# Performance work log

Hardware: AMD Instinct MI355X
Metric: run time of the kernel (lower is better)

The kernel has to match this reference:

```python
import jax, jax.numpy as jnp
import numpy as np

B, CDD, HIS, S, L, F, K = 32, 5, 100, 20, 3, 150, 18
NNEWS, RDIM = 10000, 256


def _maxpool3(x):
    # kernel [3,3,3], stride [3,3,3], no padding (torch MaxPool3d default)
    return jax.lax.reduce_window(x, -jnp.inf, jax.lax.max,
                                 (1, 1, 3, 3, 3), (1, 1, 3, 3, 3), 'VALID')


def setup_inputs() -> dict:
    key = jax.random.key(0)
    ks = jax.random.split(key, 10)
    return {
        'cdd_id': jax.random.randint(ks[0], (B, CDD), 0, NNEWS),
        'his_id': jax.random.randint(ks[1], (B, HIS), 0, NNEWS),
        'news_repr_table': jax.random.normal(ks[2], (NNEWS, RDIM), jnp.float32),
        'news_embedding_table': jax.random.normal(ks[3], (NNEWS, S * L * F), jnp.float32),
        'conv1_w': jax.random.normal(ks[4], (32, 3, 3, 3, 3), jnp.float32) * 0.1,
        'conv1_b': jax.random.normal(ks[5], (32,), jnp.float32) * 0.1,
        'conv2_w': jax.random.normal(ks[6], (16, 32, 3, 3, 3), jnp.float32) * 0.1,
        'conv2_b': jax.random.normal(ks[7], (16,), jnp.float32) * 0.1,
        'ltr_w': jax.random.normal(ks[8], (1, 128), jnp.float32) * 0.1,
        'ltr_b': jax.random.normal(ks[9], (1,), jnp.float32) * 0.1,
    }


def reference(cdd_id, his_id, news_repr_table, news_embedding_table,
              conv1_w, conv1_b, conv2_w, conv2_b, ltr_w, ltr_b):
    cdd_repr = news_repr_table[cdd_id]                    # [B,CDD,R]
    his_repr = news_repr_table[his_id]                    # [B,HIS,R]
    cdd_emb = news_embedding_table[cdd_id].reshape(B, CDD, S, L, F)
    his_emb = news_embedding_table[his_id]                # [B,HIS,S*L*F]

    # attention scores; original applies softmax then sorts the (detached)
    # weights -- softmax is monotone per row so argsort on logits is identical
    attn = jnp.einsum('bcr,bhr->bch', cdd_repr, his_repr)  # [B,CDD,HIS]
    topk_idx = jnp.argsort(-attn, axis=-1)[..., :K]        # [B,CDD,K]

    # direct gather (replaces the one_hot @ embedding matmul, same math)
    his_act = his_emb[jnp.arange(B)[:, None, None], topk_idx]  # [B,CDD,K,S*L*F]
    his_act = his_act.reshape(B, CDD, K, S, L, F)

    # fusion tensor at each dilation level
    cdd_t = cdd_emb.transpose(0, 1, 3, 2, 4)       # [B,CDD,L,S,F]
    his_t = his_act.transpose(0, 1, 2, 4, 3, 5)    # [B,CDD,K,L,S,F]
    fusion = jnp.einsum('bclsf,bckltf->bcklst', cdd_t, his_t) / np.sqrt(F).astype(np.float32)
    x = fusion.reshape(B * CDD, K, L, S, S).transpose(0, 2, 1, 3, 4)  # [B*CDD,L,K,S,S]

    dn = ('NCDHW', 'OIDHW', 'NCDHW')
    pad1 = [(1, 1)] * 3
    x = jax.lax.conv_general_dilated(x, conv1_w, (1, 1, 1), pad1, dimension_numbers=dn)
    x = jax.nn.relu(x + conv1_b[None, :, None, None, None])
    x = _maxpool3(x)                                # [B*CDD,32,6,6,6]
    x = jax.lax.conv_general_dilated(x, conv2_w, (1, 1, 1), pad1, dimension_numbers=dn)
    x = jax.nn.relu(x + conv2_b[None, :, None, None, None])
    x = _maxpool3(x)                                # [B*CDD,16,2,2,2]

    feat = x.reshape(B, CDD, -1)                    # [B,CDD,128]
    score = jnp.einsum('bcd,od->bco', feat, ltr_w)[..., 0] + ltr_b[0]  # [B,CDD]
    return jax.nn.log_softmax(score, axis=1)
```

## Files before the change

### kernel.cpp

```cpp
#include <hip/hip_runtime.h>
#include <hip/hip_bf16.h>
#include <math.h>

#define B_    32
#define CDD_  5
#define HIS_  100
#define S_    20
#define L_    3
#define F_    150
#define K_    18
#define RDIM_ 256
#define ROWE_ 9000
#define NBC_  160

__global__ __launch_bounds__(64) void attn_topk_kernel(
    const int* __restrict__ cdd_id, const int* __restrict__ his_id,
    const float* __restrict__ repr, int* __restrict__ gid,
    float* __restrict__ score) {
  int bc = blockIdx.x;
  int b  = bc / CDD_;
  int lane = threadIdx.x;
  __shared__ float cddv[RDIM_];
  int cid = cdd_id[bc];
  for (int i = lane; i < RDIM_; i += 64)
    cddv[i] = repr[(size_t)cid * RDIM_ + i];
  __syncthreads();

  float v0 = -INFINITY, v1 = -INFINITY;
  {
    const float* row = repr + (size_t)his_id[b * HIS_ + lane] * RDIM_;
    float acc = 0.f;
    for (int r = 0; r < RDIM_; r++) acc = fmaf(cddv[r], row[r], acc);
    v0 = acc;
  }
  if (lane + 64 < HIS_) {
    const float* row = repr + (size_t)his_id[b * HIS_ + lane + 64] * RDIM_;
    float acc = 0.f;
    for (int r = 0; r < RDIM_; r++) acc = fmaf(cddv[r], row[r], acc);
    v1 = acc;
  }

  for (int k = 0; k < K_; k++) {
    float bv; int bi;
    if (v1 > v0) { bv = v1; bi = lane + 64; } else { bv = v0; bi = lane; }
    #pragma unroll
    for (int off = 32; off >= 1; off >>= 1) {
      float ov = __shfl_xor(bv, off);
      int   oi = __shfl_xor(bi, off);
      if (ov > bv || (ov == bv && oi < bi)) { bv = ov; bi = oi; }
    }
    if (lane == 0) gid[bc * K_ + k] = his_id[b * HIS_ + bi];
    if (bi == lane)      v0 = -INFINITY;
    if (bi == lane + 64) v1 = -INFINITY;
  }
  if (lane == 0) score[bc] = 0.f;
}

__global__ __launch_bounds__(256) void fusion_kernel(
    const int* __restrict__ cdd_id, const int* __restrict__ gid,
    const float* __restrict__ emb, float* __restrict__ x1) {
  int bck = blockIdx.x;
  int bc = bck / K_, k = bck % K_;
  __shared__ float hs[ROWE_];
  const float* crow = emb + (size_t)cdd_id[bc] * ROWE_;
  const float4* h4 = (const float4*)(emb + (size_t)gid[bck] * ROWE_);
  float4* hs4 = (float4*)hs;
  for (int i = threadIdx.x; i < ROWE_ / 4; i += 256) hs4[i] = h4[i];
  __syncthreads();

  const float scale = 0.0816496580927726f;
  for (int tile = threadIdx.x; tile < 300; tile += 256) {
    int l = tile / 100; int rem = tile % 100;
    int s0 = (rem / 10) * 2, t0 = (rem % 10) * 2;
    const float* c0 = crow + s0 * 450 + l * 150;
    const float* c1 = c0 + 450;
    const float* h0 = hs + t0 * 450 + l * 150;
    const float* h1 = h0 + 450;
    float a00 = 0, a01 = 0, a10 = 0, a11 = 0;
    for (int f = 0; f < F_; f += 2) {
      float2 ca = *(const float2*)(c0 + f);
      float2 cb = *(const float2*)(c1 + f);
      float2 ha = *(const float2*)(h0 + f);
      float2 hb = *(const float2*)(h1 + f);
      a00 = fmaf(ca.x, ha.x, a00); a00 = fmaf(ca.y, ha.y, a00);
      a01 = fmaf(ca.x, hb.x, a01); a01 = fmaf(ca.y, hb.y, a01);
      a10 = fmaf(cb.x, ha.x, a10); a10 = fmaf(cb.y, ha.y, a10);
      a11 = fmaf(cb.x, hb.x, a11); a11 = fmaf(cb.y, hb.y, a11);
    }
    size_t base = ((size_t)(bc * 3 + l) * K_ + k) * 400 + s0 * 20 + t0;
    x1[base]      = a00 * scale;
    x1[base + 1]  = a01 * scale;
    x1[base + 20] = a10 * scale;
    x1[base + 21] = a11 * scale;
  }
}

__global__ __launch_bounds__(256) void conv1_kernel(
    const float* __restrict__ x1, const float* __restrict__ w1,
    const float* __restrict__ b1, float* __restrict__ p1) {
  int bid = blockIdx.x;
  int n = bid / 6, dp = bid % 6;
  __shared__ float tile[3 * 5 * 22 * 22];
  __shared__ unsigned pooled[32 * 36];
  int tid = threadIdx.x;

  for (int i = tid; i < 7260; i += 256) {
    int c = i / 2420; int r = i % 2420;
    int dd = r / 484; r %= 484;
    int hh = r / 22, ww = r % 22;
    int d = dp * 3 + dd - 1, h = hh - 1, w = ww - 1;
    float v = 0.f;
    if (d >= 0 && d < 18 && h >= 0 && h < 20 && w >= 0 && w < 20)
      v = x1[((size_t)(n * 3 + c) * K_ + d) * 400 + h * 20 + w];
    tile[i] = v;
  }
  for (int i = tid; i < 1152; i += 256) pooled[i] = 0u;
  __syncthreads();

  for (int pos = tid; pos < 972; pos += 256) {
    int dl = pos / 324; int r = pos % 324;
    int h = r / 18, w = r % 18;
    float in[81];
    #pragma unroll
    for (int c = 0; c < 3; c++)
      #pragma unroll
      for (int kd = 0; kd < 3; kd++)
        #pragma unroll
        for (int kh = 0; kh < 3; kh++)
          #pragma unroll
          for (int kw = 0; kw < 3; kw++)
            in[((c * 3 + kd) * 3 + kh) * 3 + kw] =
                tile[((c * 5 + dl + kd) * 22 + h + kh) * 22 + w + kw];
    int pbase = (h / 3) * 6 + (w / 3);
    for (int oc = 0; oc < 32; oc++) {
      float acc = b1[oc];
      #pragma unroll
      for (int j = 0; j < 81; j++) acc = fmaf(in[j], w1[oc * 81 + j], acc);
      acc = fmaxf(acc, 0.f);
      atomicMax(&pooled[oc * 36 + pbase], __float_as_uint(acc));
    }
  }
  __syncthreads();
  for (int i = tid; i < 1152; i += 256) {
    int oc = i / 36; int r = i % 36;
    p1[(size_t)(n * 32 + oc) * 216 + dp * 36 + r] = __uint_as_float(pooled[i]);
  }
}

__global__ __launch_bounds__(256) void conv2_kernel(
    const float* __restrict__ p1, const float* __restrict__ w2,
    const float* __restrict__ b2, const float* __restrict__ lw,
    float* __restrict__ score) {
  int bid = blockIdx.x;
  int n = bid / 2, og = bid % 2;
  __shared__ float tile[32 * 216];
  __shared__ unsigned pooled[64];
  int tid = threadIdx.x;

  for (int i = tid; i < 32 * 216; i += 256)
    tile[i] = p1[(size_t)n * 32 * 216 + i];
  if (tid < 64) pooled[tid] = 0u;
  __syncthreads();

  if (tid < 216) {
    int d = tid / 36; int r = tid % 36;
    int h = r / 6, w = r % 6;
    float acc[8];
    #pragma unroll
    for (int oc = 0; oc < 8; oc++) acc[oc] = b2[og * 8 + oc];
    for (int c = 0; c < 32; c++) {
      float win[27];
      #pragma unroll
      for (int kd = 0; kd < 3; kd++)
        #pragma unroll
        for (int kh = 0; kh < 3; kh++)
          #pragma unroll
          for (int kw = 0; kw < 3; kw++) {
            int dd = d + kd - 1, hh = h + kh - 1, ww = w + kw - 1;
            bool ok = (dd >= 0 && dd < 6 && hh >= 0 && hh < 6 && ww >= 0 && ww < 6);
            win[(kd * 3 + kh) * 3 + kw] =
                ok ? tile[c * 216 + dd * 36 + hh * 6 + ww] : 0.f;
          }
      #pragma unroll
      for (int oc = 0; oc < 8; oc++) {
        const float* wp = w2 + ((size_t)(og * 8 + oc) * 32 + c) * 27;
        #pragma unroll
        for (int j = 0; j < 27; j++) acc[oc] = fmaf(win[j], wp[j], acc[oc]);
      }
    }
    int pb = (d / 3) * 4 + (h / 3) * 2 + (w / 3);
    #pragma unroll
    for (int oc = 0; oc < 8; oc++)
      atomicMax(&pooled[oc * 8 + pb], __float_as_uint(fmaxf(acc[oc], 0.f)));
  }
  __syncthreads();

  if (tid < 64) {
    int oc = tid / 8, pb = tid % 8;
    float contrib = __uint_as_float(pooled[tid]) * lw[(og * 8 + oc) * 8 + pb];
    #pragma unroll
    for (int off = 32; off >= 1; off >>= 1) contrib += __shfl_xor(contrib, off);
    if (tid == 0) atomicAdd(&score[n], contrib);
  }
}

__global__ __launch_bounds__(64) void softmax_kernel(
    const float* __restrict__ score, const float* __restrict__ lb,
    float* __restrict__ out) {
  int b = threadIdx.x;
  if (b < B_) {
    float s[CDD_];
    float mx = -INFINITY;
    #pragma unroll
    for (int c = 0; c < CDD_; c++) {
      s[c] = score[b * CDD_ + c] + lb[0];
      mx = fmaxf(mx, s[c]);
    }
    float sum = 0.f;
    #pragma unroll
    for (int c = 0; c < CDD_; c++) sum += expf(s[c] - mx);
    float lse = mx + logf(sum);
    #pragma unroll
    for (int c = 0; c < CDD_; c++) out[b * CDD_ + c] = s[c] - lse;
  }
}

extern "C" void kernel_launch(void* const* d_in, const int* in_sizes, int n_in,
                              void* d_out, int out_size, void* d_ws, size_t ws_size,
                              hipStream_t stream) {
  const int*   cdd_id = (const int*)d_in[0];
  const int*   his_id = (const int*)d_in[1];
  const float* repr   = (const float*)d_in[2];
  const float* emb    = (const float*)d_in[3];
  const float* w1     = (const float*)d_in[4];
  const float* b1     = (const float*)d_in[5];
  const float* w2     = (const float*)d_in[6];
  const float* b2     = (const float*)d_in[7];
  const float* lw     = (const float*)d_in[8];
  const float* lb     = (const float*)d_in[9];
  float* out = (float*)d_out;

  char* ws = (char*)d_ws;
  int*   gid   = (int*)ws;
  float* score = (float*)(ws + 11520);
  float* x1    = (float*)(ws + 12160);
  float* p1    = (float*)(ws + 12160 + 13824000);

  attn_topk_kernel<<<NBC_, 64, 0, stream>>>(cdd_id, his_id, repr, gid, score);
  fusion_kernel<<<NBC_ * K_, 256, 0, stream>>>(cdd_id, gid, emb, x1);
  conv1_kernel<<<NBC_ * 6, 256, 0, stream>>>(x1, w1, b1, p1);
  conv2_kernel<<<NBC_ * 2, 256, 0, stream>>>(p1, w2, b2, lw, score);
  softmax_kernel<<<1, 64, 0, stream>>>(score, lb, out);
}
```

Measured before the change: 699.5 us.

## Transpose conv weights, reorder conv loops over output channels, parallelize attention dot products

Adds a prep kernel that transposes the conv1 and conv2 weights so the output-channel index is innermost. Conv1 now keeps 32 output accumulators per position and conv2 reads a zero-padded shared tile, so each input value is loaded once and the weights are read with uniform, contiguous loads instead of a per-channel 81-tap gather. The attention kernel now runs with four waves and does one cross-lane dot product per history item, replacing the per-thread serial 256-length loops. The cost is an extra kernel launch, more registers in conv1 (32 accumulators), and a larger shared tile in conv2.

Measured after the change: 623.5 us. 10.9% less time.

```diff
diff --git a/kernel.cpp b/kernel.cpp
--- a/kernel.cpp
+++ b/kernel.cpp
@@ -13,47 +13,65 @@
 #define ROWE_ 9000
 #define NBC_  160
 
-__global__ __launch_bounds__(64) void attn_topk_kernel(
+__global__ __launch_bounds__(256) void prep_kernel(
+    const float* __restrict__ w1, const float* __restrict__ w2,
+    float* __restrict__ w1t, float* __restrict__ w2t) {
+  int tid = blockIdx.x * 256 + threadIdx.x;
+  if (tid < 32 * 81) {
+    int oc = tid / 81, j = tid % 81;
+    w1t[j * 32 + oc] = w1[tid];
+  }
+  if (tid < 16 * 864) {
+    int oc = tid / 864, r = tid % 864;
+    w2t[r * 16 + oc] = w2[tid];
+  }
+}
+
+__global__ __launch_bounds__(256) void attn_topk_kernel(
     const int* __restrict__ cdd_id, const int* __restrict__ his_id,
     const float* __restrict__ repr, int* __restrict__ gid,
     float* __restrict__ score) {
   int bc = blockIdx.x;
   int b  = bc / CDD_;
-  int lane = threadIdx.x;
+  int tid = threadIdx.x, lane = tid & 63, wave = tid >> 6;
   __shared__ float cddv[RDIM_];
+  __shared__ float sattn[128];
   int cid = cdd_id[bc];
-  for (int i = lane; i < RDIM_; i += 64)
-    cddv[i] = repr[(size_t)cid * RDIM_ + i];
-  __syncthreads();
-
-  float v0 = -INFINITY, v1 = -INFINITY;
-  {
-    const float* row = repr + (size_t)his_id[b * HIS_ + lane] * RDIM_;
-    float acc = 0.f;
-    for (int r = 0; r < RDIM_; r++) acc = fmaf(cddv[r], row[r], acc);
-    v0 = acc;
-  }
-  if (lane + 64 < HIS_) {
-    const float* row = repr + (size_t)his_id[b * HIS_ + lane + 64] * RDIM_;
-    float acc = 0.f;
-    for (int r = 0; r < RDIM_; r++) acc = fmaf(cddv[r], row[r], acc);
-    v1 = acc;
-  }
-
-  for (int k = 0; k < K_; k++) {
-    float bv; int bi;
-    if (v1 > v0) { bv = v1; bi = lane + 64; } else { bv = v0; bi = lane; }
-    #pragma unroll
-    for (int off = 32; off >= 1; off >>= 1) {
-      float ov = __shfl_xor(bv, off);
-      int   oi = __shfl_xor(bi, off);
-      if (ov > bv || (ov == bv && oi < bi)) { bv = ov; bi = oi; }
-    }
-    if (lane == 0) gid[bc * K_ + k] = his_id[b * HIS_ + bi];
-    if (bi == lane)      v0 = -INFINITY;
-    if (bi == lane + 64) v1 = -INFINITY;
-  }
-  if (lane == 0) score[bc] = 0.f;
+  cddv[tid] = repr[(size_t)cid * RDIM_ + tid];
+  if (tid < 28) sattn[100 + tid] = -INFINITY;
+  __syncthreads();
+
+  float4 cv = *(const float4*)(cddv + lane * 4);
+  for (int h = wave; h < HIS_; h += 4) {
+    const float4* row = (const float4*)(repr + (size_t)his_id[b * HIS_ + h] * RDIM_);
+    float4 rv = row[lane];
+    float p = cv.x * rv.x;
+    p = fmaf(cv.y, rv.y, p);
+    p = fmaf(cv.z, rv.z, p);
+    p = fmaf(cv.w, rv.w, p);
+    #pragma unroll
+    for (int off = 32; off >= 1; off >>= 1) p += __shfl_xor(p, off);
+    if (lane == 0) sattn[h] = p;
+  }
+  __syncthreads();
+
+  if (wave == 0) {
+    float v0 = sattn[lane], v1 = sattn[lane + 64];
+    for (int k = 0; k < K_; k++) {
+      float bv; int bi;
+      if (v1 > v0) { bv = v1; bi = lane + 64; } else { bv = v0; bi = lane; }
+      #pragma unroll
+      for (int off = 32; off >= 1; off >>= 1) {
+        float ov = __shfl_xor(bv, off);
+        int   oi = __shfl_xor(bi, off);
+        if (ov > bv || (ov == bv && oi < bi)) { bv = ov; bi = oi; }
+      }
+      if (lane == 0) gid[bc * K_ + k] = his_id[b * HIS_ + bi];
+      if (bi == lane)      v0 = -INFINITY;
+      if (bi == lane + 64) v1 = -INFINITY;
+    }
+  }
+  if (tid == 0) score[bc] = 0.f;
 }
 
 __global__ __launch_bounds__(256) void fusion_kernel(
@@ -96,7 +114,7 @@
 }
 
 __global__ __launch_bounds__(256) void conv1_kernel(
-    const float* __restrict__ x1, const float* __restrict__ w1,
+    const float* __restrict__ x1, const float* __restrict__ w1t,
     const float* __restrict__ b1, float* __restrict__ p1) {
   int bid = blockIdx.x;
   int n = bid / 6, dp = bid % 6;
@@ -120,73 +138,79 @@
   for (int pos = tid; pos < 972; pos += 256) {
     int dl = pos / 324; int r = pos % 324;
     int h = r / 18, w = r % 18;
-    float in[81];
-    #pragma unroll
-    for (int c = 0; c < 3; c++)
-      #pragma unroll
-      for (int kd = 0; kd < 3; kd++)
-        #pragma unroll
-        for (int kh = 0; kh < 3; kh++)
-          #pragma unroll
-          for (int kw = 0; kw < 3; kw++)
-            in[((c * 3 + kd) * 3 + kh) * 3 + kw] =
-                tile[((c * 5 + dl + kd) * 22 + h + kh) * 22 + w + kw];
-    int pbase = (h / 3) * 6 + (w / 3);
-    for (int oc = 0; oc < 32; oc++) {
-      float acc = b1[oc];
-      #pragma unroll
-      for (int j = 0; j < 81; j++) acc = fmaf(in[j], w1[oc * 81 + j], acc);
-      acc = fmaxf(acc, 0.f);
-      atomicMax(&pooled[oc * 36 + pbase], __float_as_uint(acc));
-    }
-  }
-  __syncthreads();
-  for (int i = tid; i < 1152; i += 256) {
-    int oc = i / 36; int r = i % 36;
-    p1[(size_t)(n * 32 + oc) * 216 + dp * 36 + r] = __uint_as_float(pooled[i]);
-  }
-}
-
-__global__ __launch_bounds__(256) void conv2_kernel(
-    const float* __restrict__ p1, const float* __restrict__ w2,
-    const float* __restrict__ b2, const float* __restrict__ lw,
-    float* __restrict__ score) {
-  int bid = blockIdx.x;
-  int n = bid / 2, og = bid % 2;
-  __shared__ float tile[32 * 216];
-  __shared__ unsigned pooled[64];
-  int tid = threadIdx.x;
-
-  for (int i = tid; i < 32 * 216; i += 256)
-    tile[i] = p1[(size_t)n * 32 * 216 + i];
-  if (tid < 64) pooled[tid] = 0u;
-  __syncthreads();
-
-  if (tid < 216) {
-    int d = tid / 36; int r = tid % 36;
-    int h = r / 6, w = r % 6;
-    float acc[8];
-    #pragma unroll
-    for (int oc = 0; oc < 8; oc++) acc[oc] = b2[og * 8 + oc];
-    for (int c = 0; c < 32; c++) {
-      float win[27];
+    float acc[32];
+    #pragma unroll
+    for (int oc = 0; oc < 32; oc++) acc[oc] = b1[oc];
+
+    for (int c = 0; c < 3; c++) {
+      const float* tc = tile + (c * 5 + dl) * 484 + h * 22 + w;
+      const float* wc = w1t + c * 27 * 32;
       #pragma unroll
       for (int kd = 0; kd < 3; kd++)
         #pragma unroll
         for (int kh = 0; kh < 3; kh++)
           #pragma unroll
           for (int kw = 0; kw < 3; kw++) {
-            int dd = d + kd - 1, hh = h + kh - 1, ww = w + kw - 1;
-            bool ok = (dd >= 0 && dd < 6 && hh >= 0 && hh < 6 && ww >= 0 && ww < 6);
-            win[(kd * 3 + kh) * 3 + kw] =
-                ok ? tile[c * 216 + dd * 36 + hh * 6 + ww] : 0.f;
+            float iv = tc[kd * 484 + kh * 22 + kw];
+            const float* wp = wc + (kd * 9 + kh * 3 + kw) * 32;
+            #pragma unroll
+            for (int oc = 0; oc < 32; oc++) acc[oc] = fmaf(iv, wp[oc], acc[oc]);
           }
+    }
+    int pbase = (h / 3) * 6 + (w / 3);
+    #pragma unroll
+    for (int oc = 0; oc < 32; oc++)
+      atomicMax(&pooled[oc * 36 + pbase], __float_as_uint(fmaxf(acc[oc], 0.f)));
+  }
+  __syncthreads();
+  for (int i = tid; i < 1152; i += 256) {
+    int oc = i / 36; int r = i % 36;
+    p1[(size_t)(n * 32 + oc) * 216 + dp * 36 + r] = __uint_as_float(pooled[i]);
+  }
+}
+
+__global__ __launch_bounds__(256) void conv2_kernel(
+    const float* __restrict__ p1, const float* __restrict__ w2t,
+    const float* __restrict__ b2, const float* __restrict__ lw,
+    float* __restrict__ score) {
+  int bid = blockIdx.x;
+  int n = bid / 2, og = bid % 2;
+  __shared__ float tile[32 * 8 * 8 * 8];
+  __shared__ unsigned pooled[64];
+  int tid = threadIdx.x;
+
+  for (int i = tid; i < 32 * 512; i += 256) tile[i] = 0.f;
+  if (tid < 64) pooled[tid] = 0u;
+  __syncthreads();
+  for (int i = tid; i < 32 * 216; i += 256) {
+    int c = i / 216; int r = i % 216;
+    int d = r / 36; r %= 36;
+    int h = r / 6, w = r % 6;
+    tile[c * 512 + (d + 1) * 64 + (h + 1) * 8 + (w + 1)] =
+        p1[(size_t)n * 32 * 216 + i];
+  }
+  __syncthreads();
+
+  if (tid < 216) {
+    int d = tid / 36; int r = tid % 36;
+    int h = r / 6, w = r % 6;
+    float acc[8];
+    #pragma unroll
+    for (int oc = 0; oc < 8; oc++) acc[oc] = b2[og * 8 + oc];
+    for (int c = 0; c < 32; c++) {
+      const float* tc = tile + c * 512 + d * 64 + h * 8 + w;
+      const float* wc = w2t + c * 27 * 16 + og * 8;
       #pragma unroll
-      for (int oc = 0; oc < 8; oc++) {
-        const float* wp = w2 + ((size_t)(og * 8 + oc) * 32 + c) * 27;
+      for (int kd = 0; kd < 3; kd++)
         #pragma unroll
-        for (int j = 0; j < 27; j++) acc[oc] = fmaf(win[j], wp[j], acc[oc]);
-      }
+        for (int kh = 0; kh < 3; kh++)
+          #pragma unroll
+          for (int kw = 0; kw < 3; kw++) {
+            float iv = tc[kd * 64 + kh * 8 + kw];
+            const float* wp = wc + (kd * 9 + kh * 3 + kw) * 16;
+            #pragma unroll
+            for (int oc = 0; oc < 8; oc++) acc[oc] = fmaf(iv, wp[oc], acc[oc]);
+          }
     }
     int pb = (d / 3) * 4 + (h / 3) * 2 + (w / 3);
     #pragma unroll
@@ -245,10 +269,13 @@
   float* score = (float*)(ws + 11520);
   float* x1    = (float*)(ws + 12160);
   float* p1    = (float*)(ws + 12160 + 13824000);
-
-  attn_topk_kernel<<<NBC_, 64, 0, stream>>>(cdd_id, his_id, repr, gid, score);
+  float* w1t   = (float*)(ws + 12160 + 13824000 + 4423680);
+  float* w2t   = (float*)(ws + 12160 + 13824000 + 4423680 + 10368);
+
+  prep_kernel<<<54, 256, 0, stream>>>(w1, w2, w1t, w2t);
+  attn_topk_kernel<<<NBC_, 256, 0, stream>>>(cdd_id, his_id, repr, gid, score);
   fusion_kernel<<<NBC_ * K_, 256, 0, stream>>>(cdd_id, gid, emb, x1);
-  conv1_kernel<<<NBC_ * 6, 256, 0, stream>>>(x1, w1, b1, p1);
-  conv2_kernel<<<NBC_ * 2, 256, 0, stream>>>(p1, w2, b2, lw, score);
+  conv1_kernel<<<NBC_ * 6, 256, 0, stream>>>(x1, w1t, b1, p1);
+  conv2_kernel<<<NBC_ * 2, 256, 0, stream>>>(p1, w2t, b2, lw, score);
   softmax_kernel<<<1, 64, 0, stream>>>(score, lb, out);
 }
```
